# Performance work log

Hardware: AMD Instinct MI355X
Metric: run time of the kernel (lower is better)

## Reference

```python
import jax, jax.numpy as jnp
import numpy as np

L, S, N, E, H = 2048, 2048, 4, 1024, 16
HD = E // H  # head_dim = 64


def setup_inputs() -> dict:
    key = jax.random.key(0)
    ks = jax.random.split(key, 7)
    sc = 0.02
    return {
        "query": jax.random.normal(ks[0], (L, N, E), dtype=jnp.float32),
        "key": jax.random.normal(ks[1], (S, N, E), dtype=jnp.float32),
        "value": jax.random.normal(ks[2], (S, N, E), dtype=jnp.float32),
        "in_proj_weight": jax.random.normal(ks[3], (3 * E, E), dtype=jnp.float32) * sc,
        "in_proj_bias": jax.random.normal(ks[4], (3 * E,), dtype=jnp.float32) * sc,
        "out_proj_weight": jax.random.normal(ks[5], (E, E), dtype=jnp.float32) * sc,
        "out_proj_bias": jax.random.normal(ks[6], (E,), dtype=jnp.float32) * sc,
    }


def reference(query, key, value, in_proj_weight, in_proj_bias, out_proj_weight, out_proj_bias):
    # in_proj_weight is [3E, E]; torch slices it into q/k/v projections.
    w_q, w_k, w_v = in_proj_weight[:E], in_proj_weight[E:2 * E], in_proj_weight[2 * E:]
    b_q, b_k, b_v = in_proj_bias[:E], in_proj_bias[E:2 * E], in_proj_bias[2 * E:]
    scaling = float(HD) ** -0.5

    q = (query @ w_q.T + b_q) * scaling          # (L, N, E), scaled as in torch
    k = key @ w_k.T + b_k                        # (S, N, E)
    v = value @ w_v.T + b_v                      # (S, N, E)

    q = q.reshape(L, N, H, HD)
    k = k.reshape(S, N, H, HD)
    v = v.reshape(S, N, H, HD)

    # full L x S attention scores per (batch, head) — the naive pre-fused path
    scores = jnp.einsum("lnhd,snhd->nhls", q, k)         # (N, H, L, S)
    attn = jax.nn.softmax(scores, axis=-1)               # (N, H, L, S)
    # dropout_p = 0.0 -> no dropout

    ctx = jnp.einsum("nhls,snhd->lnhd", attn, v).reshape(L, N, E)
    attn_output = ctx @ out_proj_weight.T + out_proj_bias  # (L, N, E)

    # need_weights=True: average attention weights over heads -> (N, L, S)
    attn_output_weights = jnp.sum(attn, axis=1) / H
    return attn_output, attn_output_weights
```

## Files before the change

### kernel.cpp

```cpp
#include <hip/hip_runtime.h>

using f32x4  = __attribute__((ext_vector_type(4))) float;
using short8 = __attribute__((ext_vector_type(8))) short;
using short4v = __attribute__((ext_vector_type(4))) short;

__device__ __forceinline__ short f2bf(float f) {
  unsigned u = __float_as_uint(f);
  u += 0x7fffu + ((u >> 16) & 1u);
  return (short)(u >> 16);
}

__device__ __forceinline__ void async16(const void* g, void* l) {
  __builtin_amdgcn_global_load_lds(
      (const __attribute__((address_space(1))) unsigned int*)g,
      (__attribute__((address_space(3))) unsigned int*)l, 16, 0, 0);
}

__global__ void __launch_bounds__(256) cvt_kernel(const float* __restrict__ src,
                                                  short* __restrict__ dst,
                                                  int permute) {
  const int r = blockIdx.x;
  const int t = threadIdx.x;
  int srcRow = r;
  if (permute) { int n = r >> 11; int l = r & 2047; srcRow = l * 4 + n; }
  float4 v = *(const float4*)(src + (size_t)srcRow * 1024 + t * 4);
  short4v o;
  o.x = f2bf(v.x); o.y = f2bf(v.y); o.z = f2bf(v.z); o.w = f2bf(v.w);
  *(short4v*)(dst + (size_t)r * 1024 + t * 4) = o;
}

template <bool F32OUT>
__global__ void __launch_bounds__(256) gemm_bt(const short* __restrict__ A0,
                                               const short* __restrict__ B0,
                                               const float* __restrict__ bias0,
                                               void* __restrict__ out0,
                                               long zA, long zB, long zBias, long zOut,
                                               float scale0) {
  __shared__ short As[128 * 32];
  __shared__ short Bs[128 * 32];
  const int bz = blockIdx.z;
  const short* A = A0 + (size_t)bz * zA;
  const short* B = B0 + (size_t)bz * zB;
  const float* bias = bias0 + (size_t)bz * zBias;
  const float scale = (bz == 0) ? scale0 : 1.0f;

  const int t = threadIdx.x;
  const int wave = t >> 6, lane = t & 63;
  const int quad = lane >> 4, li = lane & 15;
  const int wm = wave >> 1, wn = wave & 1;
  const int bm = blockIdx.y, bn = blockIdx.x;
  const short* Ablk = A + (size_t)bm * 128 * 1024;
  const short* Bblk = B + (size_t)bn * 128 * 1024;

  float bv[4];
#pragma unroll
  for (int nt = 0; nt < 4; nt++) bv[nt] = bias[bn * 128 + wn * 64 + nt * 16 + li];

  f32x4 acc[4][4];
#pragma unroll
  for (int mt = 0; mt < 4; mt++)
#pragma unroll
    for (int nt = 0; nt < 4; nt++) acc[mt][nt] = (f32x4){0.f, 0.f, 0.f, 0.f};

  for (int kk = 0; kk < 32; kk++) {
    const int k0 = kk * 32;
    __syncthreads();
#pragma unroll
    for (int r = 0; r < 2; r++) {
      int idx = r * 256 + t;
      int row = idx >> 2, pos = idx & 3;
      int c = pos ^ ((row >> 1) & 3);
      async16(Ablk + (size_t)row * 1024 + k0 + c * 8, &As[idx * 8]);
    }
#pragma unroll
    for (int r = 0; r < 2; r++) {
      int idx = r * 256 + t;
      int row = idx >> 2, pos = idx & 3;
      int c = pos ^ ((row >> 1) & 3);
      async16(Bblk + (size_t)row * 1024 + k0 + c * 8, &Bs[idx * 8]);
    }
    __syncthreads();

    short8 af[4], bf[4];
#pragma unroll
    for (int mt = 0; mt < 4; mt++) {
      int m = wm * 64 + mt * 16 + li;
      int pos = quad ^ ((m >> 1) & 3);
      af[mt] = *(const short8*)&As[m * 32 + pos * 8];
    }
#pragma unroll
    for (int nt = 0; nt < 4; nt++) {
      int nn = wn * 64 + nt * 16 + li;
      int pos = quad ^ ((nn >> 1) & 3);
      bf[nt] = *(const short8*)&Bs[nn * 32 + pos * 8];
    }
#pragma unroll
    for (int mt = 0; mt < 4; mt++)
#pragma unroll
      for (int nt = 0; nt < 4; nt++)
        acc[mt][nt] = __builtin_amdgcn_mfma_f32_16x16x32_bf16(af[mt], bf[nt], acc[mt][nt], 0, 0, 0);
  }

#pragma unroll
  for (int mt = 0; mt < 4; mt++)
#pragma unroll
    for (int nt = 0; nt < 4; nt++) {
      int cg = bn * 128 + wn * 64 + nt * 16 + li;
#pragma unroll
      for (int rr = 0; rr < 4; rr++) {
        int rg = bm * 128 + wm * 64 + mt * 16 + quad * 4 + rr;
        float v = (acc[mt][nt][rr] + bv[nt]) * scale;
        if (F32OUT)
          ((float*)out0)[(size_t)bz * zOut + (size_t)rg * 1024 + cg] = v;
        else
          ((short*)out0)[(size_t)bz * zOut + (size_t)rg * 1024 + cg] = f2bf(v);
      }
    }
}

__global__ void __launch_bounds__(256) vtrans(const short* __restrict__ V,
                                              short* __restrict__ Vt) {
  __shared__ short tile[64][72];
  const int e0 = blockIdx.x * 64;
  const int s0 = blockIdx.y * 64;
  const int n = blockIdx.z;
  const int t = threadIdx.x;
#pragma unroll
  for (int r = 0; r < 2; r++) {
    int idx = r * 256 + t;
    int srow = idx >> 3, c = idx & 7;
    short8 v = *(const short8*)(V + (size_t)(n * 2048 + s0 + srow) * 1024 + e0 + c * 8);
    *(short8*)&tile[srow][c * 8] = v;
  }
  __syncthreads();
#pragma unroll
  for (int r = 0; r < 2; r++) {
    int idx = r * 256 + t;
    int erow = idx >> 3, c = idx & 7;
    short8 o;
#pragma unroll
    for (int j = 0; j < 8; j++) o[j] = tile[c * 8 + j][erow];
    *(short8*)(Vt + (size_t)(n * 1024 + e0 + erow) * 2048 + s0 + c * 8) = o;
  }
}

__global__ void __launch_bounds__(512, 4) attn_ctx(const short* __restrict__ Qws,
                                                   const short* __restrict__ Kws,
                                                   const short* __restrict__ Vtws,
                                                   short* __restrict__ Ctx,
                                                   float* __restrict__ Rden) {
  __shared__ short Ks[64 * 64];
  __shared__ short Vs[64 * 64];
  __shared__ short et[8][16][68];

  const int bid = blockIdx.x;
  const int h = bid & 15;
  const int n = (bid >> 4) & 3;
  const int lc = bid >> 6;
  const int t = threadIdx.x;
  const int wave = t >> 6, lane = t & 63;
  const int quad = lane >> 4, li = lane & 15;
  const int sw = li & 7;
  const int l0 = lc * 128 + wave * 16;

  const size_t Kn = (size_t)n * 2048 * 1024;
  const size_t Vnb = ((size_t)n * 1024 + h * 64) * 2048;

  short8 qf0 = *(const short8*)(Qws + Kn + (size_t)(l0 + li) * 1024 + h * 64 + quad * 8);
  short8 qf1 = *(const short8*)(Qws + Kn + (size_t)(l0 + li) * 1024 + h * 64 + 32 + quad * 8);

  const int srow = lane >> 3;
  const int c = lane & 7;
  const int row8 = wave * 8 + srow;
  const int gch = c ^ (row8 & 7);
  const short* gK = Kws + Kn + (size_t)row8 * 1024 + h * 64 + gch * 8;
  const short* gV = Vtws + Vnb + (size_t)row8 * 2048 + gch * 8;
  short* lK = &Ks[0] + wave * 512 + lane * 8;
  short* lV = &Vs[0] + wave * 512 + lane * 8;

  f32x4 ctx[4];
  f32x4 den = (f32x4){0.f, 0.f, 0.f, 0.f};
#pragma unroll
  for (int nt = 0; nt < 4; nt++) ctx[nt] = (f32x4){0.f, 0.f, 0.f, 0.f};

  for (int it = 0; it < 32; it++) {
    __syncthreads();
    async16(gK, lK);
    async16(gV, lV);
    gK += 64 * 1024;
    gV += 64;
    __syncthreads();

    f32x4 sc[4];
#pragma unroll
    for (int nts = 0; nts < 4; nts++) sc[nts] = (f32x4){0.f, 0.f, 0.f, 0.f};
#pragma unroll
    for (int nts = 0; nts < 4; nts++) {
      const int row = nts * 16 + li;
      short8 k0 = *(const short8*)&Ks[row * 64 + ((quad ^ sw) << 3)];
      short8 k1 = *(const short8*)&Ks[row * 64 + (((4 + quad) ^ sw) << 3)];
      sc[nts] = __builtin_amdgcn_mfma_f32_16x16x32_bf16(qf0, k0, sc[nts], 0, 0, 0);
      sc[nts] = __builtin_amdgcn_mfma_f32_16x16x32_bf16(qf1, k1, sc[nts], 0, 0, 0);
    }
#pragma unroll
    for (int nts = 0; nts < 4; nts++)
#pragma unroll
      for (int rr = 0; rr < 4; rr++) {
        float e = __expf(sc[nts][rr]);
        den[rr] += e;
        et[wave][quad * 4 + rr][nts * 16 + li] = f2bf(e);
      }
    asm volatile("s_waitcnt lgkmcnt(0)" ::: "memory");
    short8 e0 = *(const short8*)&et[wave][li][quad * 8];
    short8 e1 = *(const short8*)&et[wave][li][32 + quad * 8];
#pragma unroll
    for (int nt = 0; nt < 4; nt++) {
      const int row = nt * 16 + li;
      short8 v0 = *(const short8*)&Vs[row * 64 + ((quad ^ sw) << 3)];
      short8 v1 = *(const short8*)&Vs[row * 64 + (((4 + quad) ^ sw) << 3)];
      ctx[nt] = __builtin_amdgcn_mfma_f32_16x16x32_bf16(e0, v0, ctx[nt], 0, 0, 0);
      ctx[nt] = __builtin_amdgcn_mfma_f32_16x16x32_bf16(e1, v1, ctx[nt], 0, 0, 0);
    }
  }

#pragma unroll
  for (int off = 1; off < 16; off <<= 1)
#pragma unroll
    for (int rr = 0; rr < 4; rr++) den[rr] += __shfl_xor(den[rr], off);
  f32x4 rden;
#pragma unroll
  for (int rr = 0; rr < 4; rr++) rden[rr] = 1.0f / den[rr];

  if (li == 0) {
#pragma unroll
    for (int rr = 0; rr < 4; rr++)
      Rden[((size_t)n * 16 + h) * 2048 + l0 + quad * 4 + rr] = rden[rr];
  }

#pragma unroll
  for (int nt = 0; nt < 4; nt++)
#pragma unroll
    for (int rr = 0; rr < 4; rr++) {
      int l = l0 + quad * 4 + rr;
      float v = ctx[nt][rr] * rden[rr];
      Ctx[((size_t)l * 4 + n) * 1024 + h * 64 + nt * 16 + li] = f2bf(v);
    }
}

__global__ void __launch_bounds__(512, 2) attn_w(const short* __restrict__ Qws,
                                                 const short* __restrict__ Kws,
                                                 const float* __restrict__ Rden,
                                                 float* __restrict__ Wout) {
  __shared__ short Qs[128 * 64];
  __shared__ short Ks2[128 * 64];
  __shared__ __align__(16) float rl[16][128];

  const int bid = blockIdx.x;
  const int xcd = bid & 7;
  const int n = xcd >> 1;
  const int u = ((bid >> 3) << 1) | (xcd & 1);
  const int lt = u >> 4;
  const int st = u & 15;
  const int l0 = lt * 128;
  const int s0 = st * 128;
  const int t = threadIdx.x;
  const int wave = t >> 6, lane = t & 63;
  const int quad = lane >> 4, li = lane & 15;
  const int wm = wave >> 2, wn = wave & 3;

  const size_t Kn = (size_t)n * 2048 * 1024;
  const short* Qg = Qws + Kn + (size_t)l0 * 1024;
  const short* Kg = Kws + Kn + (size_t)s0 * 1024;

  {
    int idx = t * 4;
    int hh = idx >> 7, ll = idx & 127;
    *(float4*)&rl[hh][ll] =
        *(const float4*)(Rden + ((size_t)n * 16 + hh) * 2048 + l0 + ll);
  }

  f32x4 ws[4][2];
#pragma unroll
  for (int mt = 0; mt < 4; mt++)
#pragma unroll
    for (int st2 = 0; st2 < 2; st2++) ws[mt][st2] = (f32x4){0.f, 0.f, 0.f, 0.f};

  for (int h = 0; h < 16; h++) {
    __syncthreads();
#pragma unroll
    for (int r = 0; r < 2; r++) {
      int idx = r * 512 + t;
      int row = idx >> 3, pos = idx & 7;
      int c = pos ^ (row & 7);
      async16(Qg + (size_t)row * 1024 + h * 64 + c * 8, &Qs[idx * 8]);
    }
#pragma unroll
    for (int r = 0; r < 2; r++) {
      int idx = r * 512 + t;
      int row = idx >> 3, pos = idx & 7;
      int c = pos ^ (row & 7);
      async16(Kg + (size_t)row * 1024 + h * 64 + c * 8, &Ks2[idx * 8]);
    }
    __syncthreads();

    f32x4 sc[4][2];
#pragma unroll
    for (int mt = 0; mt < 4; mt++)
#pragma unroll
      for (int st2 = 0; st2 < 2; st2++) sc[mt][st2] = (f32x4){0.f, 0.f, 0.f, 0.f};

#pragma unroll
    for (int kh = 0; kh < 2; kh++) {
      short8 af[4], bf[2];
#pragma unroll
      for (int mt = 0; mt < 4; mt++) {
        int m = wm * 64 + mt * 16 + li;
        int ch = (kh * 4 + quad) ^ (m & 7);
        af[mt] = *(const short8*)&Qs[m * 64 + ch * 8];
      }
#pragma unroll
      for (int st2 = 0; st2 < 2; st2++) {
        int s = wn * 32 + st2 * 16 + li;
        int ch = (kh * 4 + quad) ^ (s & 7);
        bf[st2] = *(const short8*)&Ks2[s * 64 + ch * 8];
      }
#pragma unroll
      for (int mt = 0; mt < 4; mt++)
#pragma unroll
        for (int st2 = 0; st2 < 2; st2++)
          sc[mt][st2] = __builtin_amdgcn_mfma_f32_16x16x32_bf16(af[mt], bf[st2],
                                                                sc[mt][st2], 0, 0, 0);
    }

#pragma unroll
    for (int mt = 0; mt < 4; mt++) {
      f32x4 rd = *(const f32x4*)&rl[h][wm * 64 + mt * 16 + quad * 4];
#pragma unroll
      for (int st2 = 0; st2 < 2; st2++)
#pragma unroll
        for (int rr = 0; rr < 4; rr++)
          ws[mt][st2][rr] += __expf(sc[mt][st2][rr]) * rd[rr];
    }
  }

#pragma unroll
  for (int mt = 0; mt < 4; mt++)
#pragma unroll
    for (int st2 = 0; st2 < 2; st2++)
#pragma unroll
      for (int rr = 0; rr < 4; rr++) {
        int rg = l0 + wm * 64 + mt * 16 + quad * 4 + rr;
        int cg = s0 + wn * 32 + st2 * 16 + li;
        Wout[((size_t)n * 2048 + rg) * 2048 + cg] = ws[mt][st2][rr] * 0.0625f;
      }
}

extern "C" void kernel_launch(void* const* d_in, const int* in_sizes, int n_in,
                              void* d_out, int out_size, void* d_ws, size_t ws_size,
                              hipStream_t stream) {
  (void)in_sizes; (void)n_in; (void)out_size; (void)ws_size;
  const float* query = (const float*)d_in[0];
  const float* key_  = (const float*)d_in[1];
  const float* value = (const float*)d_in[2];
  const float* ipw   = (const float*)d_in[3];
  const float* ipb   = (const float*)d_in[4];
  const float* opw   = (const float*)d_in[5];
  const float* opb   = (const float*)d_in[6];
  float* out = (float*)d_out;
  char* ws = (char*)d_ws;
  const size_t MB = 1024 * 1024;

  short* Xq  = (short*)(ws + 0 * MB);
  short* Xk  = (short*)(ws + 16 * MB);
  short* Xv  = (short*)(ws + 32 * MB);
  short* Wb  = (short*)(ws + 48 * MB);
  short* Wob = (short*)(ws + 54 * MB);
  short* Qw  = (short*)(ws + 56 * MB);
  short* Kw  = (short*)(ws + 72 * MB);
  short* Vw  = (short*)(ws + 88 * MB);
  short* Vt  = Xk;
  short* Ctx = Xq;
  float* Rden = (float*)Xv;

  cvt_kernel<<<dim3(8192), dim3(256), 0, stream>>>(query, Xq, 1);
  cvt_kernel<<<dim3(8192), dim3(256), 0, stream>>>(key_,  Xk, 1);
  cvt_kernel<<<dim3(8192), dim3(256), 0, stream>>>(value, Xv, 1);
  cvt_kernel<<<dim3(3072), dim3(256), 0, stream>>>(ipw, Wb,  0);
  cvt_kernel<<<dim3(1024), dim3(256), 0, stream>>>(opw, Wob, 0);

  gemm_bt<false><<<dim3(8, 64, 3), dim3(256), 0, stream>>>(
      Xq, Wb, ipb, (void*)Qw, (long)8192 * 1024, (long)1024 * 1024, 1024,
      (long)8192 * 1024, 0.125f);

  vtrans<<<dim3(16, 32, 4), dim3(256), 0, stream>>>(Vw, Vt);

  attn_ctx<<<dim3(1024), dim3(512), 0, stream>>>(Qw, Kw, Vt, Ctx, Rden);
  attn_w<<<dim3(1024), dim3(512), 0, stream>>>(Qw, Kw, Rden, out + 8388608);

  gemm_bt<true><<<dim3(8, 64, 1), dim3(256), 0, stream>>>(
      Ctx, Wob, opb, (void*)out, 0, 0, 0, 0, 1.0f);
}
```

Before: 457.3 us.

## Double-buffer K/V and Q/K LDS tiles in attention kernels to overlap loads

Both attention kernels, attn_ctx and attn_w, now keep two LDS buffers per operand. The next tile's async global-to-LDS load is issued right after a barrier, and the current tile is computed while that load is in flight. This hides load latency behind MFMA and exp work instead of stalling at a barrier on every iteration. The cost is double the LDS for these tiles, which may lower how many blocks fit per CU, especially for attn_ctx, which was tuned for four blocks.

New measurement: 471.1 us. 1.03x slower.

```diff
diff --git a/kernel.cpp b/kernel.cpp
--- a/kernel.cpp
+++ b/kernel.cpp
@@ -149,8 +149,10 @@
                                                    const short* __restrict__ Vtws,
                                                    short* __restrict__ Ctx,
                                                    float* __restrict__ Rden) {
-  __shared__ short Ks[64 * 64];
-  __shared__ short Vs[64 * 64];
+  __shared__ short Ks0[64 * 64];
+  __shared__ short Ks1[64 * 64];
+  __shared__ short Vs0[64 * 64];
+  __shared__ short Vs1[64 * 64];
   __shared__ short et[8][16][68];
 
   const int bid = blockIdx.x;
@@ -175,53 +177,57 @@
   const int gch = c ^ (row8 & 7);
   const short* gK = Kws + Kn + (size_t)row8 * 1024 + h * 64 + gch * 8;
   const short* gV = Vtws + Vnb + (size_t)row8 * 2048 + gch * 8;
-  short* lK = &Ks[0] + wave * 512 + lane * 8;
-  short* lV = &Vs[0] + wave * 512 + lane * 8;
+  short* lK0 = &Ks0[0] + wave * 512 + lane * 8;
+  short* lK1 = &Ks1[0] + wave * 512 + lane * 8;
+  short* lV0 = &Vs0[0] + wave * 512 + lane * 8;
+  short* lV1 = &Vs1[0] + wave * 512 + lane * 8;
 
   f32x4 ctx[4];
   f32x4 den = (f32x4){0.f, 0.f, 0.f, 0.f};
 #pragma unroll
   for (int nt = 0; nt < 4; nt++) ctx[nt] = (f32x4){0.f, 0.f, 0.f, 0.f};
 
-  for (int it = 0; it < 32; it++) {
-    __syncthreads();
-    async16(gK, lK);
-    async16(gV, lV);
-    gK += 64 * 1024;
-    gV += 64;
-    __syncthreads();
-
-    f32x4 sc[4];
-#pragma unroll
-    for (int nts = 0; nts < 4; nts++) sc[nts] = (f32x4){0.f, 0.f, 0.f, 0.f};
-#pragma unroll
-    for (int nts = 0; nts < 4; nts++) {
-      const int row = nts * 16 + li;
-      short8 k0 = *(const short8*)&Ks[row * 64 + ((quad ^ sw) << 3)];
-      short8 k1 = *(const short8*)&Ks[row * 64 + (((4 + quad) ^ sw) << 3)];
-      sc[nts] = __builtin_amdgcn_mfma_f32_16x16x32_bf16(qf0, k0, sc[nts], 0, 0, 0);
-      sc[nts] = __builtin_amdgcn_mfma_f32_16x16x32_bf16(qf1, k1, sc[nts], 0, 0, 0);
-    }
-#pragma unroll
-    for (int nts = 0; nts < 4; nts++)
-#pragma unroll
-      for (int rr = 0; rr < 4; rr++) {
-        float e = __expf(sc[nts][rr]);
-        den[rr] += e;
-        et[wave][quad * 4 + rr][nts * 16 + li] = f2bf(e);
-      }
-    asm volatile("s_waitcnt lgkmcnt(0)" ::: "memory");
-    short8 e0 = *(const short8*)&et[wave][li][quad * 8];
-    short8 e1 = *(const short8*)&et[wave][li][32 + quad * 8];
-#pragma unroll
-    for (int nt = 0; nt < 4; nt++) {
-      const int row = nt * 16 + li;
-      short8 v0 = *(const short8*)&Vs[row * 64 + ((quad ^ sw) << 3)];
-      short8 v1 = *(const short8*)&Vs[row * 64 + (((4 + quad) ^ sw) << 3)];
-      ctx[nt] = __builtin_amdgcn_mfma_f32_16x16x32_bf16(e0, v0, ctx[nt], 0, 0, 0);
-      ctx[nt] = __builtin_amdgcn_mfma_f32_16x16x32_bf16(e1, v1, ctx[nt], 0, 0, 0);
-    }
-  }
+#define CTX_COMPUTE(KS, VS) do {                                               \
+    f32x4 sc[4];                                                               \
+    _Pragma("unroll") for (int nts = 0; nts < 4; nts++)                        \
+        sc[nts] = (f32x4){0.f, 0.f, 0.f, 0.f};                                 \
+    _Pragma("unroll") for (int nts = 0; nts < 4; nts++) {                      \
+      const int row = nts * 16 + li;                                           \
+      short8 k0 = *(const short8*)&KS[row * 64 + ((quad ^ sw) << 3)];          \
+      short8 k1 = *(const short8*)&KS[row * 64 + (((4 + quad) ^ sw) << 3)];    \
+      sc[nts] = __builtin_amdgcn_mfma_f32_16x16x32_bf16(qf0, k0, sc[nts], 0, 0, 0); \
+      sc[nts] = __builtin_amdgcn_mfma_f32_16x16x32_bf16(qf1, k1, sc[nts], 0, 0, 0); \
+    }                                                                          \
+    _Pragma("unroll") for (int nts = 0; nts < 4; nts++)                        \
+      _Pragma("unroll") for (int rr = 0; rr < 4; rr++) {                       \
+        float e = __expf(sc[nts][rr]);                                         \
+        den[rr] += e;                                                          \
+        et[wave][quad * 4 + rr][nts * 16 + li] = f2bf(e);                      \
+      }                                                                        \
+    asm volatile("s_waitcnt lgkmcnt(0)" ::: "memory");                         \
+    short8 e0 = *(const short8*)&et[wave][li][quad * 8];                       \
+    short8 e1 = *(const short8*)&et[wave][li][32 + quad * 8];                  \
+    _Pragma("unroll") for (int nt = 0; nt < 4; nt++) {                         \
+      const int row = nt * 16 + li;                                            \
+      short8 v0 = *(const short8*)&VS[row * 64 + ((quad ^ sw) << 3)];          \
+      short8 v1 = *(const short8*)&VS[row * 64 + (((4 + quad) ^ sw) << 3)];    \
+      ctx[nt] = __builtin_amdgcn_mfma_f32_16x16x32_bf16(e0, v0, ctx[nt], 0, 0, 0); \
+      ctx[nt] = __builtin_amdgcn_mfma_f32_16x16x32_bf16(e1, v1, ctx[nt], 0, 0, 0); \
+    }                                                                          \
+  } while (0)
+
+  async16(gK, lK0); async16(gV, lV0);
+  gK += 64 * 1024; gV += 64;
+
+  for (int it = 0; it < 32; it += 2) {
+    __syncthreads();
+    if (it + 1 < 32) { async16(gK, lK1); async16(gV, lV1); gK += 64 * 1024; gV += 64; }
+    CTX_COMPUTE(Ks0, Vs0);
+    __syncthreads();
+    if (it + 2 < 32) { async16(gK, lK0); async16(gV, lV0); gK += 64 * 1024; gV += 64; }
+    CTX_COMPUTE(Ks1, Vs1);
+  }
+#undef CTX_COMPUTE
 
 #pragma unroll
   for (int off = 1; off < 16; off <<= 1)
@@ -251,8 +257,10 @@
                                                  const short* __restrict__ Kws,
                                                  const float* __restrict__ Rden,
                                                  float* __restrict__ Wout) {
-  __shared__ short Qs[128 * 64];
-  __shared__ short Ks2[128 * 64];
+  __shared__ short Qs0[128 * 64];
+  __shared__ short Qs1[128 * 64];
+  __shared__ short Ks20[128 * 64];
+  __shared__ short Ks21[128 * 64];
   __shared__ __align__(16) float rl[16][128];
 
   const int bid = blockIdx.x;
@@ -285,63 +293,63 @@
 #pragma unroll
     for (int st2 = 0; st2 < 2; st2++) ws[mt][st2] = (f32x4){0.f, 0.f, 0.f, 0.f};
 
-  for (int h = 0; h < 16; h++) {
-    __syncthreads();
-#pragma unroll
-    for (int r = 0; r < 2; r++) {
-      int idx = r * 512 + t;
-      int row = idx >> 3, pos = idx & 7;
-      int c = pos ^ (row & 7);
-      async16(Qg + (size_t)row * 1024 + h * 64 + c * 8, &Qs[idx * 8]);
-    }
-#pragma unroll
-    for (int r = 0; r < 2; r++) {
-      int idx = r * 512 + t;
-      int row = idx >> 3, pos = idx & 7;
-      int c = pos ^ (row & 7);
-      async16(Kg + (size_t)row * 1024 + h * 64 + c * 8, &Ks2[idx * 8]);
-    }
-    __syncthreads();
-
-    f32x4 sc[4][2];
-#pragma unroll
-    for (int mt = 0; mt < 4; mt++)
-#pragma unroll
-      for (int st2 = 0; st2 < 2; st2++) sc[mt][st2] = (f32x4){0.f, 0.f, 0.f, 0.f};
-
-#pragma unroll
-    for (int kh = 0; kh < 2; kh++) {
-      short8 af[4], bf[2];
-#pragma unroll
-      for (int mt = 0; mt < 4; mt++) {
-        int m = wm * 64 + mt * 16 + li;
-        int ch = (kh * 4 + quad) ^ (m & 7);
-        af[mt] = *(const short8*)&Qs[m * 64 + ch * 8];
-      }
-#pragma unroll
-      for (int st2 = 0; st2 < 2; st2++) {
-        int s = wn * 32 + st2 * 16 + li;
-        int ch = (kh * 4 + quad) ^ (s & 7);
-        bf[st2] = *(const short8*)&Ks2[s * 64 + ch * 8];
-      }
-#pragma unroll
-      for (int mt = 0; mt < 4; mt++)
-#pragma unroll
-        for (int st2 = 0; st2 < 2; st2++)
-          sc[mt][st2] = __builtin_amdgcn_mfma_f32_16x16x32_bf16(af[mt], bf[st2],
-                                                                sc[mt][st2], 0, 0, 0);
-    }
-
-#pragma unroll
-    for (int mt = 0; mt < 4; mt++) {
-      f32x4 rd = *(const f32x4*)&rl[h][wm * 64 + mt * 16 + quad * 4];
-#pragma unroll
-      for (int st2 = 0; st2 < 2; st2++)
-#pragma unroll
-        for (int rr = 0; rr < 4; rr++)
-          ws[mt][st2][rr] += __expf(sc[mt][st2][rr]) * rd[rr];
-    }
-  }
+#define AW_STAGE(QS, KS, H) do {                                               \
+    _Pragma("unroll") for (int r = 0; r < 2; r++) {                            \
+      int idx = r * 512 + t;                                                   \
+      int row = idx >> 3, pos = idx & 7;                                       \
+      int cc = pos ^ (row & 7);                                                \
+      async16(Qg + (size_t)row * 1024 + (H) * 64 + cc * 8, &QS[idx * 8]);      \
+    }                                                                          \
+    _Pragma("unroll") for (int r = 0; r < 2; r++) {                            \
+      int idx = r * 512 + t;                                                   \
+      int row = idx >> 3, pos = idx & 7;                                       \
+      int cc = pos ^ (row & 7);                                                \
+      async16(Kg + (size_t)row * 1024 + (H) * 64 + cc * 8, &KS[idx * 8]);      \
+    }                                                                          \
+  } while (0)
+
+#define AW_COMPUTE(QS, KS, H) do {                                             \
+    f32x4 sc[4][2];                                                            \
+    _Pragma("unroll") for (int mt = 0; mt < 4; mt++)                           \
+      _Pragma("unroll") for (int st2 = 0; st2 < 2; st2++)                      \
+          sc[mt][st2] = (f32x4){0.f, 0.f, 0.f, 0.f};                           \
+    _Pragma("unroll") for (int kh = 0; kh < 2; kh++) {                         \
+      short8 af[4], bf[2];                                                     \
+      _Pragma("unroll") for (int mt = 0; mt < 4; mt++) {                       \
+        int m = wm * 64 + mt * 16 + li;                                        \
+        int ch = (kh * 4 + quad) ^ (m & 7);                                    \
+        af[mt] = *(const short8*)&QS[m * 64 + ch * 8];                         \
+      }                                                                        \
+      _Pragma("unroll") for (int st2 = 0; st2 < 2; st2++) {                    \
+        int s = wn * 32 + st2 * 16 + li;                                       \
+        int ch = (kh * 4 + quad) ^ (s & 7);                                    \
+        bf[st2] = *(const short8*)&KS[s * 64 + ch * 8];                        \
+      }                                                                        \
+      _Pragma("unroll") for (int mt = 0; mt < 4; mt++)                         \
+        _Pragma("unroll") for (int st2 = 0; st2 < 2; st2++)                    \
+            sc[mt][st2] = __builtin_amdgcn_mfma_f32_16x16x32_bf16(             \
+                af[mt], bf[st2], sc[mt][st2], 0, 0, 0);                        \
+    }                                                                          \
+    _Pragma("unroll") for (int mt = 0; mt < 4; mt++) {                         \
+      f32x4 rd = *(const f32x4*)&rl[(H)][wm * 64 + mt * 16 + quad * 4];        \
+      _Pragma("unroll") for (int st2 = 0; st2 < 2; st2++)                      \
+        _Pragma("unroll") for (int rr = 0; rr < 4; rr++)                       \
+            ws[mt][st2][rr] += __expf(sc[mt][st2][rr]) * rd[rr];               \
+    }                                                                          \
+  } while (0)
+
+  AW_STAGE(Qs0, Ks20, 0);
+
+  for (int h = 0; h < 16; h += 2) {
+    __syncthreads();
+    if (h + 1 < 16) AW_STAGE(Qs1, Ks21, h + 1);
+    AW_COMPUTE(Qs0, Ks20, h);
+    __syncthreads();
+    if (h + 2 < 16) AW_STAGE(Qs0, Ks20, h + 2);
+    AW_COMPUTE(Qs1, Ks21, h + 1);
+  }
+#undef AW_STAGE
+#undef AW_COMPUTE
 
 #pragma unroll
   for (int mt = 0; mt < 4; mt++)
```
